# Optimization experiments

Measured on AMD Instinct MI355X. Metric: run time of the kernel, lower is better.

The kernel has to match this reference:

```python
import jax, jax.numpy as jnp
import numpy as np

N_NODES = 50000
N_EDGES = 600000
D_IN, D_H1, D_H2 = 128, 128, 64


def setup_inputs() -> dict:
    key = jax.random.key(0)
    ks = jax.random.split(key, 8)
    x = jax.random.normal(ks[0], (N_NODES, D_IN), dtype=jnp.float32)
    edge_index = jax.random.randint(ks[1], (2, N_EDGES), 0, N_NODES, dtype=jnp.int64)
    # Glorot-style init for GCN weights, uniform for biases
    W1 = jax.random.normal(ks[2], (D_IN, D_H1), dtype=jnp.float32) / np.sqrt(D_IN)
    b1 = jnp.zeros((D_H1,), dtype=jnp.float32)
    W2 = jax.random.normal(ks[3], (D_H1, D_H2), dtype=jnp.float32) / np.sqrt(D_H1)
    b2 = jnp.zeros((D_H2,), dtype=jnp.float32)
    W3 = jax.random.normal(ks[4], (D_H2, 1), dtype=jnp.float32) / np.sqrt(D_H2)
    b3 = jnp.zeros((1,), dtype=jnp.float32)
    return {"x": x, "edge_index": edge_index, "W1": W1, "b1": b1,
            "W2": W2, "b2": b2, "W3": W3, "b3": b3}


def _gcn_norm(edge_index, n_nodes, dtype):
    # Add self-loops, then symmetric normalization deg^-1/2 * deg^-1/2 (PyG gcn_norm).
    loop = jnp.arange(n_nodes, dtype=edge_index.dtype)
    src = jnp.concatenate([edge_index[0], loop])
    dst = jnp.concatenate([edge_index[1], loop])
    deg = jax.ops.segment_sum(jnp.ones_like(dst, dtype=dtype), dst, num_segments=n_nodes)
    dinv = jnp.where(deg > 0, jax.lax.rsqrt(deg), 0.0)
    norm = dinv[src] * dinv[dst]  # [E+N]
    return src, dst, norm


def _gcn_conv(x, src, dst, norm, W, b, n_nodes):
    h = x @ W                       # [N, F_out]
    msg = h[src] * norm[:, None]    # gather + scale: [E+N, F_out]
    out = jax.ops.segment_sum(msg, dst, num_segments=n_nodes)  # scatter-add
    return out + b


def reference(x, edge_index, W1, b1, W2, b2, W3, b3):
    n = x.shape[0]
    src, dst, norm = _gcn_norm(edge_index, n, x.dtype)
    h = jax.nn.relu(_gcn_conv(x, src, dst, norm, W1, b1, n))
    # dropout is identity in eval mode
    h = jax.nn.relu(_gcn_conv(h, src, dst, norm, W2, b2, n))
    return h @ W3 + b3  # [N, 1]
```

## Files before the change

kernel.cpp:

```cpp
#include <hip/hip_runtime.h>

#define N_NODES 50000
#define N_EDGES 600000
#define CAP 64
#define GB1 ((N_NODES + 63) / 64)
#define FB  ((N_EDGES + 255) / 256)
#define ZB  ((12500 + 255) / 256)

typedef unsigned int u32;
typedef unsigned short u16;
typedef __attribute__((ext_vector_type(8))) short short8;
typedef __attribute__((ext_vector_type(4))) float f32x4;

__device__ __forceinline__ u16 f2bf(float f) {
    u32 u = __float_as_uint(f);
    u32 r = (u + 0x7fffu + ((u >> 16) & 1u)) >> 16;
    return (u16)r;
}
__device__ __forceinline__ float bf_lo(u32 u) { return __uint_as_float(u << 16); }
__device__ __forceinline__ float bf_hi(u32 u) { return __uint_as_float(u & 0xffff0000u); }


__global__ __launch_bounds__(256) void init_k(int* __restrict__ deg,
                                              const float* __restrict__ W1,
                                              const float* __restrict__ W2,
                                              u16* __restrict__ W1t,
                                              u16* __restrict__ W2t) {
    int b = blockIdx.x, t = threadIdx.x;
    if (b < ZB) {
        int i = b * 256 + t;
        if (i < 12500) ((int4*)deg)[i] = make_int4(0, 0, 0, 0);
    } else if (b < ZB + 64) {
        int i = (b - ZB) * 256 + t;
        int n = i >> 7, k = i & 127;
        W1t[i] = f2bf(W1[k * 128 + n]);
    } else {
        int j = (b - ZB - 64) * 256 + t;
        int n = j >> 7, k = j & 127;
        W2t[j] = f2bf(W2[k * 64 + n]);
    }
}


#define SL 136

__global__ __launch_bounds__(256) void gemm1_count(const float* __restrict__ A,
                                                   const u16* __restrict__ Bt,
                                                   u16* __restrict__ out,
                                                   const int* __restrict__ ei,
                                                   int* __restrict__ deg,
                                                   int* __restrict__ col) {
    __shared__ u16 As[64 * SL];
    __shared__ u16 Bs[128 * SL];
    const int tid = threadIdx.x;
    const int b = blockIdx.x;
    if (b >= GB1) {
        int e = (b - GB1) * 256 + tid;
        if (e < N_EDGES) {
            int s = ei[e];
            int d = ei[N_EDGES + e];
            int r = atomicAdd(&deg[d], 1);
            if (r < CAP) col[((size_t)d << 6) + r] = s;
        }
        return;
    }
    const int m0 = b * 64;
    {
        int row = tid >> 2, c0 = (tid & 3) * 32;
        bool ok = (m0 + row) < N_NODES;
        const float4* src = (const float4*)&A[(size_t)(m0 + row) * 128 + c0];
        u16* dst = &As[row * SL + c0];
#pragma unroll
        for (int i = 0; i < 8; ++i) {
            float4 v = ok ? src[i] : make_float4(0.f, 0.f, 0.f, 0.f);
            u32 lo = (u32)f2bf(v.x) | ((u32)f2bf(v.y) << 16);
            u32 hi = (u32)f2bf(v.z) | ((u32)f2bf(v.w) << 16);
            *(uint2*)&dst[i * 4] = make_uint2(lo, hi);
        }
    }
    {
        int n = tid >> 1, h = (tid & 1) * 64;
        const uint4* src = (const uint4*)&Bt[n * 128 + h];
        u16* dst = &Bs[n * SL + h];
#pragma unroll
        for (int i = 0; i < 8; ++i) *(uint4*)&dst[i * 8] = src[i];
    }
    __syncthreads();

    const int l = tid & 63, w = tid >> 6;
    const int q = l >> 4, r16 = l & 15;
    const int m_off = w * 16;
    f32x4 acc[8] = {};
#pragma unroll
    for (int kt = 0; kt < 128; kt += 32) {
        short8 a = *(const short8*)&As[(m_off + r16) * SL + kt + q * 8];
        short8 bb[8];
#pragma unroll
        for (int tn = 0; tn < 8; ++tn)
            bb[tn] = *(const short8*)&Bs[(tn * 16 + r16) * SL + kt + q * 8];
#pragma unroll
        for (int tn = 0; tn < 8; ++tn)
            acc[tn] = __builtin_amdgcn_mfma_f32_16x16x32_bf16(a, bb[tn], acc[tn], 0, 0, 0);
    }
#pragma unroll
    for (int r = 0; r < 4; ++r) {
        int row = m0 + m_off + q * 4 + r;
        if (row < N_NODES) {
#pragma unroll
            for (int tn = 0; tn < 8; ++tn)
                out[(size_t)row * 128 + tn * 16 + r16] = f2bf(acc[tn][r]);
        }
    }
}


__global__ __launch_bounds__(256) void agg_gemm2(const u16* __restrict__ hs,
                                                 const int* __restrict__ deg,
                                                 const int* __restrict__ col,
                                                 const float* __restrict__ bias,
                                                 const u16* __restrict__ Bt,
                                                 u16* __restrict__ out) {
    __shared__ u16 As[64 * SL];
    __shared__ u16 Bs[64 * SL];
    const int tid = threadIdx.x;
    const int m0 = blockIdx.x * 64;
    {
        int n = tid >> 2, s0 = (tid & 3) * 32;
        const uint4* src = (const uint4*)&Bt[n * 128 + s0];
        u16* dst = &Bs[n * SL + s0];
#pragma unroll
        for (int i = 0; i < 4; ++i) *(uint4*)&dst[i * 8] = src[i];
    }
    const uint4* rows = (const uint4*)hs;
    const int lane = tid & 15;
    const int sub = lane & 7;
    const int fo = lane * 8;
#pragma unroll
    for (int p = 0; p < 4; ++p) {
        int nl = p * 16 + (tid >> 4);
        int node = m0 + nl;
        uint4 pk = make_uint4(0, 0, 0, 0);
        if (node < N_NODES) {
            int dg = deg[node];
            float dv = rsqrtf((float)(dg + 1));
            float acc[8];
            uint4 sv = rows[(size_t)node * 16 + lane];
            acc[0] = dv * bf_lo(sv.x); acc[1] = dv * bf_hi(sv.x);
            acc[2] = dv * bf_lo(sv.y); acc[3] = dv * bf_hi(sv.y);
            acc[4] = dv * bf_lo(sv.z); acc[5] = dv * bf_hi(sv.z);
            acc[6] = dv * bf_lo(sv.w); acc[7] = dv * bf_hi(sv.w);
            const int* crow = col + ((size_t)node << 6);
            int c = crow[sub];
            c = (sub < dg) ? c : 0;
            float scr = rsqrtf((float)(deg[c] + 1));
            float sc = (sub < dg) ? scr : 0.f;
            for (int r0 = 0; r0 < dg; r0 += 8) {
                int jn = r0 + 8 + sub;
                int cn = crow[jn & (CAP - 1)];
                cn = (jn < dg) ? cn : 0;
                float scnr = rsqrtf((float)(deg[cn] + 1));
                float scn = (jn < dg) ? scnr : 0.f;
#pragma unroll
                for (int jj = 0; jj < 8; ++jj) {
                    int cj = __shfl(c, jj, 16);
                    float scj = __shfl(sc, jj, 16);
                    uint4 v = rows[(size_t)cj * 16 + lane];
                    acc[0] = fmaf(scj, bf_lo(v.x), acc[0]);
                    acc[1] = fmaf(scj, bf_hi(v.x), acc[1]);
                    acc[2] = fmaf(scj, bf_lo(v.y), acc[2]);
                    acc[3] = fmaf(scj, bf_hi(v.y), acc[3]);
                    acc[4] = fmaf(scj, bf_lo(v.z), acc[4]);
                    acc[5] = fmaf(scj, bf_hi(v.z), acc[5]);
                    acc[6] = fmaf(scj, bf_lo(v.w), acc[6]);
                    acc[7] = fmaf(scj, bf_hi(v.w), acc[7]);
                }
                c = cn; sc = scn;
            }
            u32 w0[4];
#pragma unroll
            for (int jq = 0; jq < 4; ++jq) {
                u16 a = f2bf(fmaxf(fmaf(dv, acc[2 * jq], bias[fo + 2 * jq]), 0.f));
                u16 bq = f2bf(fmaxf(fmaf(dv, acc[2 * jq + 1], bias[fo + 2 * jq + 1]), 0.f));
                w0[jq] = (u32)a | ((u32)bq << 16);
            }
            pk = make_uint4(w0[0], w0[1], w0[2], w0[3]);
        }
        *(uint4*)&As[nl * SL + fo] = pk;
    }
    __syncthreads();

    const int l = tid & 63, w = tid >> 6;
    const int q = l >> 4, r16 = l & 15;
    const int m_off = w * 16;
    f32x4 acc2[4] = {};
#pragma unroll
    for (int kt = 0; kt < 128; kt += 32) {
        short8 a = *(const short8*)&As[(m_off + r16) * SL + kt + q * 8];
        short8 bb[4];
#pragma unroll
        for (int tn = 0; tn < 4; ++tn)
            bb[tn] = *(const short8*)&Bs[(tn * 16 + r16) * SL + kt + q * 8];
#pragma unroll
        for (int tn = 0; tn < 4; ++tn)
            acc2[tn] = __builtin_amdgcn_mfma_f32_16x16x32_bf16(a, bb[tn], acc2[tn], 0, 0, 0);
    }
#pragma unroll
    for (int r = 0; r < 4; ++r) {
        int row = m0 + m_off + q * 4 + r;
        if (row < N_NODES) {
            float dvr = rsqrtf((float)(deg[row] + 1));
#pragma unroll
            for (int tn = 0; tn < 4; ++tn)
                out[(size_t)row * 64 + tn * 16 + r16] = f2bf(acc2[tn][r] * dvr);
        }
    }
}


__global__ __launch_bounds__(256) void agg_final_bf(const u16* __restrict__ hs,
                                                    const int* __restrict__ deg,
                                                    const int* __restrict__ col,
                                                    const float* __restrict__ b2,
                                                    const float* __restrict__ W3,
                                                    const float* __restrict__ b3,
                                                    float* __restrict__ out) {
    int node = blockIdx.x * 32 + (threadIdx.x >> 3);
    int lane = threadIdx.x & 7;
    if (node >= N_NODES) return;
    const uint4* rows = (const uint4*)hs;
    int dg = deg[node];
    float acc[8] = {};
    auto accum = [&](uint4 v) {
        acc[0] += bf_lo(v.x); acc[1] += bf_hi(v.x);
        acc[2] += bf_lo(v.y); acc[3] += bf_hi(v.y);
        acc[4] += bf_lo(v.z); acc[5] += bf_hi(v.z);
        acc[6] += bf_lo(v.w); acc[7] += bf_hi(v.w);
    };
    accum(rows[(size_t)node * 8 + lane]);
    const int* crow = col + ((size_t)node << 6);
    int c = crow[lane];
    c = (lane < dg) ? c : 0;
    for (int r0 = 0; r0 < dg; r0 += 8) {
        int jn = r0 + 8 + lane;
        int cn = crow[jn & (CAP - 1)];
        cn = (jn < dg) ? cn : 0;
#pragma unroll
        for (int jj = 0; jj < 8; ++jj) {
            int cj = __shfl(c, jj, 8);
            uint4 v = rows[(size_t)cj * 8 + lane];
            uint4 vv = (r0 + jj < dg) ? v : make_uint4(0, 0, 0, 0);
            accum(vv);
        }
        c = cn;
    }
    float dv = rsqrtf((float)(dg + 1));
    int fo = lane * 8;
    float vsum = 0.f;
#pragma unroll
    for (int jq = 0; jq < 8; ++jq)
        vsum += fmaxf(fmaf(dv, acc[jq], b2[fo + jq]), 0.f) * W3[fo + jq];
#pragma unroll
    for (int m = 4; m > 0; m >>= 1) vsum += __shfl_xor(vsum, m, 64);
    if (lane == 0) out[node] = vsum + b3[0];
}


extern "C" void kernel_launch(void* const* d_in, const int* in_sizes, int n_in,
                              void* d_out, int out_size, void* d_ws, size_t ws_size,
                              hipStream_t stream) {
    const float* x  = (const float*)d_in[0];
    const int*   ei = (const int*)d_in[1];
    const float* W1 = (const float*)d_in[2];
    const float* b1 = (const float*)d_in[3];
    const float* W2 = (const float*)d_in[4];
    const float* b2 = (const float*)d_in[5];
    const float* W3 = (const float*)d_in[6];
    const float* b3 = (const float*)d_in[7];
    float* out = (float*)d_out;

    char* ws = (char*)d_ws;
    size_t off = 0;
    auto alloc = [&](size_t bytes) -> void* {
        void* p = ws + off;
        off = (off + bytes + 255) & ~(size_t)255;
        return p;
    };
    int* deg = (int*)alloc(N_NODES * sizeof(int));
    int* col = (int*)alloc(((size_t)N_NODES * CAP + 64) * sizeof(int));
    u16* W1t = (u16*)alloc(128 * 128 * sizeof(u16));
    u16* W2t = (u16*)alloc(64 * 128 * sizeof(u16));
    u16* hs1 = (u16*)alloc((size_t)N_NODES * 128 * sizeof(u16));
    u16* hs2 = (u16*)alloc((size_t)N_NODES * 64 * sizeof(u16));

    init_k<<<ZB + 96, 256, 0, stream>>>(deg, W1, W2, W1t, W2t);
    gemm1_count<<<GB1 + FB, 256, 0, stream>>>(x, W1t, hs1, ei, deg, col);
    agg_gemm2<<<(N_NODES + 63) / 64, 256, 0, stream>>>(hs1, deg, col, b1, W2t, hs2);
    agg_final_bf<<<(N_NODES + 31) / 32, 256, 0, stream>>>(hs2, deg, col, b2, W3, b3, out);
}
```

Measured before the change: 182.8 us.

## Split edge fill from GEMM1 and zero degrees with memset

```diff
diff --git a/kernel.cpp b/kernel.cpp
--- a/kernel.cpp
+++ b/kernel.cpp
@@ -5,7 +5,6 @@
 #define CAP 64
 #define GB1 ((N_NODES + 63) / 64)
 #define FB  ((N_EDGES + 255) / 256)
-#define ZB  ((12500 + 255) / 256)
 
 typedef unsigned int u32;
 typedef unsigned short u16;
@@ -21,50 +20,43 @@
 __device__ __forceinline__ float bf_hi(u32 u) { return __uint_as_float(u & 0xffff0000u); }
 
 
-__global__ __launch_bounds__(256) void init_k(int* __restrict__ deg,
-                                              const float* __restrict__ W1,
-                                              const float* __restrict__ W2,
-                                              u16* __restrict__ W1t,
-                                              u16* __restrict__ W2t) {
+__global__ __launch_bounds__(256) void fill_transpose(const int* __restrict__ ei,
+                                                      int* __restrict__ deg,
+                                                      int* __restrict__ col,
+                                                      const float* __restrict__ W1,
+                                                      const float* __restrict__ W2,
+                                                      u16* __restrict__ W1t,
+                                                      u16* __restrict__ W2t) {
     int b = blockIdx.x, t = threadIdx.x;
-    if (b < ZB) {
-        int i = b * 256 + t;
-        if (i < 12500) ((int4*)deg)[i] = make_int4(0, 0, 0, 0);
-    } else if (b < ZB + 64) {
-        int i = (b - ZB) * 256 + t;
-        int n = i >> 7, k = i & 127;
-        W1t[i] = f2bf(W1[k * 128 + n]);
-    } else {
-        int j = (b - ZB - 64) * 256 + t;
-        int n = j >> 7, k = j & 127;
-        W2t[j] = f2bf(W2[k * 64 + n]);
-    }
-}
-
-
-#define SL 136
-
-__global__ __launch_bounds__(256) void gemm1_count(const float* __restrict__ A,
-                                                   const u16* __restrict__ Bt,
-                                                   u16* __restrict__ out,
-                                                   const int* __restrict__ ei,
-                                                   int* __restrict__ deg,
-                                                   int* __restrict__ col) {
-    __shared__ u16 As[64 * SL];
-    __shared__ u16 Bs[128 * SL];
-    const int tid = threadIdx.x;
-    const int b = blockIdx.x;
-    if (b >= GB1) {
-        int e = (b - GB1) * 256 + tid;
+    if (b < FB) {
+        int e = b * 256 + t;
         if (e < N_EDGES) {
             int s = ei[e];
             int d = ei[N_EDGES + e];
             int r = atomicAdd(&deg[d], 1);
             if (r < CAP) col[((size_t)d << 6) + r] = s;
         }
-        return;
-    }
-    const int m0 = b * 64;
+    } else if (b < FB + 64) {
+        int i = (b - FB) * 256 + t;
+        int n = i >> 7, k = i & 127;
+        W1t[i] = f2bf(W1[k * 128 + n]);
+    } else {
+        int j = (b - FB - 64) * 256 + t;
+        int n = j >> 7, k = j & 127;
+        W2t[j] = f2bf(W2[k * 64 + n]);
+    }
+}
+
+
+#define SL 136
+
+__global__ __launch_bounds__(256) void gemm1_k(const float* __restrict__ A,
+                                               const u16* __restrict__ Bt,
+                                               u16* __restrict__ out) {
+    __shared__ u16 As[64 * SL];
+    __shared__ u16 Bs[128 * SL];
+    const int tid = threadIdx.x;
+    const int m0 = blockIdx.x * 64;
     {
         int row = tid >> 2, c0 = (tid & 3) * 32;
         bool ok = (m0 + row) < N_NODES;
@@ -292,8 +284,9 @@
     u16* hs1 = (u16*)alloc((size_t)N_NODES * 128 * sizeof(u16));
     u16* hs2 = (u16*)alloc((size_t)N_NODES * 64 * sizeof(u16));
 
-    init_k<<<ZB + 96, 256, 0, stream>>>(deg, W1, W2, W1t, W2t);
-    gemm1_count<<<GB1 + FB, 256, 0, stream>>>(x, W1t, hs1, ei, deg, col);
+    hipMemsetAsync(deg, 0, N_NODES * sizeof(int), stream);
+    fill_transpose<<<FB + 96, 256, 0, stream>>>(ei, deg, col, W1, W2, W1t, W2t);
+    gemm1_k<<<GB1, 256, 0, stream>>>(x, W1t, hs1);
     agg_gemm2<<<(N_NODES + 63) / 64, 256, 0, stream>>>(hs1, deg, col, b1, W2t, hs2);
     agg_final_bf<<<(N_NODES + 31) / 32, 256, 0, stream>>>(hs2, deg, col, b2, W3, b3, out);
 }
```

Measured after the change: 168.1 us. 1.09x faster.
